# Performance work log

Hardware: AMD Instinct MI355X
Metric: run time of the kernel (lower is better)

The kernel has to match this reference:

```python
import jax, jax.numpy as jnp
import numpy as np

B, T, S = 64, 128, 128
E, H, D, K = 512, 1024, 1024, 1024  # embed, hidden, decoder_size, encoder.output_size
IN2 = 2 * D + 2 * H  # output_rnn input size


def gru_cell(x, h, Wih, Whh, bih, bhh):
    # PyTorch GRUCell math; gate order (r, z, n)
    gi = x @ Wih.T + bih
    gh = h @ Whh.T + bhh
    i_r, i_z, i_n = jnp.split(gi, 3, axis=-1)
    h_r, h_z, h_n = jnp.split(gh, 3, axis=-1)
    r = jax.nn.sigmoid(i_r + h_r)
    z = jax.nn.sigmoid(i_z + h_z)
    n = jnp.tanh(i_n + r * h_n)
    return (1.0 - z) * n + z * h


def setup_inputs() -> dict:
    key = jax.random.key(0)
    ks = jax.random.split(key, 24)
    p = 0.05
    rn = lambda k, s, sc=1.0: jax.random.normal(k, s, jnp.float32) * sc
    return {
        'reversed_input': rn(ks[0], (B, T, E)),
        'y_length': jnp.full((B,), T, jnp.int32),
        'mask': jnp.ones((B, T), bool),
        'y_states': rn(ks[1], (B, T, D)),
        'encoder_output': rn(ks[2], (B, S, K)),
        'src_mask': jnp.ones((B, 1, S), bool),
        # backward-reading GRU (self.rnn)
        'rnn_Wih': rn(ks[3], (3 * H, E), p), 'rnn_Whh': rn(ks[4], (3 * H, H), p),
        'rnn_bih': rn(ks[5], (3 * H,), p), 'rnn_bhh': rn(ks[6], (3 * H,), p),
        # output_rnn GRU
        'out_Wih': rn(ks[7], (3 * H, IN2), p), 'out_Whh': rn(ks[8], (3 * H, H), p),
        'out_bih': rn(ks[9], (3 * H,), p), 'out_bhh': rn(ks[10], (3 * H,), p),
        'corr_W': rn(ks[11], (D, H), p), 'corr_b': rn(ks[12], (D,), p),
        'reward_W': rn(ks[13], (2, H), p), 'reward_b': rn(ks[14], (2,), p),
        'attv_W': rn(ks[15], (H, H + K), p), 'attv_b': rn(ks[16], (H,), p),
        # Bahdanau attention (bias-free linears)
        'key_W': rn(ks[17], (H, K), p), 'query_W': rn(ks[18], (H, H), p),
        'energy_W': rn(ks[19], (1, H), p),
    }


def reference(reversed_input, y_length, mask, y_states, encoder_output, src_mask,
              rnn_Wih, rnn_Whh, rnn_bih, rnn_bhh,
              out_Wih, out_Whh, out_bih, out_bhh,
              corr_W, corr_b, reward_W, reward_b,
              attv_W, attv_b, key_W, query_W, energy_W):
    b, t, _ = reversed_input.shape
    h_dim = rnn_Whh.shape[1]
    d_dim = corr_W.shape[0]
    dt = reversed_input.dtype

    # _apply_rnn: step-by-step GRU over reversed input == full GRU scan
    def rnn_step(h, x):
        h = gru_cell(x, h, rnn_Wih, rnn_Whh, rnn_bih, rnn_bhh)
        return h, h
    h0 = jnp.zeros((b, h_dim), dt)
    _, rnn_outs = jax.lax.scan(rnn_step, h0, reversed_input.transpose(1, 0, 2))
    rnn_outputs = jnp.flip(rnn_outs.transpose(1, 0, 2), axis=1)  # [B,T,H]

    proj_keys = encoder_output @ key_W.T  # [B,S,H] precomputed attention keys
    comb_states = jnp.concatenate([y_states, rnn_outputs], axis=-1)  # [B,T,D+H]
    sm = src_mask[:, 0, :]  # [B,S]

    def step(carry, comb_t):
        h, corr_prev, att_prev = carry
        inp = jnp.concatenate([comb_t, corr_prev, att_prev], axis=-1)  # [B,2D+2H]
        h = gru_cell(inp, h, out_Wih, out_Whh, out_bih, out_bhh)  # rnn_output == hidden[-1]
        corr = jnp.tanh(h @ corr_W.T + corr_b)  # corr_activation=tanh
        reward = h @ reward_W.T + reward_b  # [B,2]
        reward_pred = jax.lax.stop_gradient(jnp.argmax(reward, axis=-1)).astype(dt)[:, None]
        # Bahdanau attention: v^T tanh(Wq q + Wk k)
        pq = h @ query_W.T  # [B,H]
        energies = jnp.tanh(pq[:, None, :] + proj_keys) @ energy_W[0]  # [B,S]
        scores = jnp.where(sm, energies, -jnp.inf)
        alphas = jax.nn.softmax(scores, axis=-1)
        context = jnp.einsum('bs,bsk->bk', alphas, encoder_output)
        att_vec = jnp.tanh(jnp.concatenate([h, context], axis=-1) @ attv_W.T + attv_b)
        corr = corr * (1.0 - reward_pred)
        return (h, corr, att_vec), (corr, reward, alphas)

    init = (jnp.zeros((b, h_dim), dt), jnp.zeros((b, d_dim), dt), jnp.zeros((b, h_dim), dt))
    _, (corrs, rewards, attns) = jax.lax.scan(step, init, comb_states.transpose(1, 0, 2))
    return (corrs.transpose(1, 0, 2), rewards.transpose(1, 0, 2), attns.transpose(1, 0, 2))
```

## Files before the change

kernel.cpp:

```cpp
#include <hip/hip_runtime.h>
#include <hip/hip_bf16.h>
#include <math.h>

#define B 64
#define T 128
#define S 128
#define E 512
#define H 1024
#define D 1024
#define KDIM 1024
#define G3 3072
#define JT 16

__device__ __forceinline__ float sigmoidf_(float x) { return 1.f / (1.f + expf(-x)); }

struct SBSeg { const float* A; const float* W; int lda; int ldw; int N; int colOff; };
struct SBArgs { SBSeg s[6]; };

__global__ __launch_bounds__(256) void sb_gemm(SBArgs args, int jtPerSeg, int Nstr,
                                               float* __restrict__ part) {
  const int seg = blockIdx.x / jtPerSeg;
  const int jt = blockIdx.x % jtPerSeg;
  const SBSeg sg = args.s[seg];
  const int j0 = jt * JT;
  if (j0 >= sg.N) return;
  const int wv = __builtin_amdgcn_readfirstlane(threadIdx.x >> 6);
  const int lane = threadIdx.x & 63;

  float a[128];
  const float4* ap = (const float4*)(sg.A + (size_t)lane * sg.lda + wv * 128);
#pragma unroll
  for (int q = 0; q < 32; ++q) {
    float4 v = ap[q];
    a[q * 4 + 0] = v.x; a[q * 4 + 1] = v.y; a[q * 4 + 2] = v.z; a[q * 4 + 3] = v.w;
  }
  float acc[JT];
#pragma unroll
  for (int jj = 0; jj < JT; ++jj) acc[jj] = 0.f;
#pragma unroll
  for (int jj = 0; jj < JT; ++jj) {
    int j = j0 + jj;
    if (j < sg.N) {
      const float4* wp = (const float4*)(sg.W + (size_t)j * sg.ldw + wv * 128);
      float s0 = 0.f, s1 = 0.f, s2 = 0.f, s3 = 0.f;
#pragma unroll
      for (int q = 0; q < 32; ++q) {
        float4 w4 = wp[q];
        s0 = fmaf(a[q * 4 + 0], w4.x, s0);
        s1 = fmaf(a[q * 4 + 1], w4.y, s1);
        s2 = fmaf(a[q * 4 + 2], w4.z, s2);
        s3 = fmaf(a[q * 4 + 3], w4.w, s3);
      }
      acc[jj] = (s0 + s1) + (s2 + s3);
    }
  }
  __shared__ float red[4][JT][64];
#pragma unroll
  for (int jj = 0; jj < JT; ++jj) red[wv][jj][lane] = acc[jj];
  __syncthreads();
  for (int idx = threadIdx.x; idx < JT * 64; idx += 256) {
    int jj = idx >> 6, b = idx & 63;
    int j = j0 + jj;
    if (j < sg.N) {
      float v = red[0][jj][b] + red[1][jj][b] + red[2][jj][b] + red[3][jj][b];
      part[((size_t)seg * Nstr + sg.colOff + j) * 64 + b] = v;
    }
  }
}

__global__ __launch_bounds__(256) void gru_reduce(
    const float* __restrict__ part, const float* __restrict__ pre_t,
    int giPlanes, int ghStart, int ghPlanes, const float* __restrict__ bhh,
    float* __restrict__ hrow, int hstride, float* __restrict__ flip_out, int t) {
  const int j0 = blockIdx.x * 4;
  const int jj = threadIdx.x >> 6;
  const int b = threadIdx.x & 63;
  const int j = j0 + jj;
  float gir = pre_t[(size_t)j * 64 + b];
  float giz = pre_t[(size_t)(H + j) * 64 + b];
  float gin = pre_t[(size_t)(2 * H + j) * 64 + b];
  for (int p2 = 0; p2 < giPlanes; ++p2) {
    const float* pp = part + (size_t)p2 * G3 * 64;
    gir += pp[(size_t)j * 64 + b];
    giz += pp[(size_t)(H + j) * 64 + b];
    gin += pp[(size_t)(2 * H + j) * 64 + b];
  }
  float ghr = bhh[j], ghz = bhh[H + j], ghn = bhh[2 * H + j];
  for (int p2 = ghStart; p2 < ghStart + ghPlanes; ++p2) {
    const float* pp = part + (size_t)p2 * G3 * 64;
    ghr += pp[(size_t)j * 64 + b];
    ghz += pp[(size_t)(H + j) * 64 + b];
    ghn += pp[(size_t)(2 * H + j) * 64 + b];
  }
  float r = sigmoidf_(gir + ghr);
  float z = sigmoidf_(giz + ghz);
  float n = tanhf(gin + r * ghn);
  float hold = hrow[(size_t)b * hstride + j];
  float hnew = (1.f - z) * n + z * hold;
  __shared__ float st[4][64];
  st[jj][b] = hnew;
  __syncthreads();
  int jl = threadIdx.x & 3, b2 = threadIdx.x >> 2;
  float v = st[jl][b2];
  hrow[(size_t)b2 * hstride + j0 + jl] = v;
  if (flip_out)
    flip_out[(size_t)b2 * T * H + (size_t)(T - 1 - t) * H + j0 + jl] = v;
}

__global__ __launch_bounds__(256) void hproj_reduce(
    const float* __restrict__ part, const float* __restrict__ corr_b,
    const float* __restrict__ reward_b, float* __restrict__ corrT,
    float* __restrict__ rewT, float* __restrict__ pq,
    float* __restrict__ out_rewards, int t) {
  const int j0 = blockIdx.x * 4;
  const int jj = threadIdx.x >> 6;
  const int b = threadIdx.x & 63;
  const int j = j0 + jj;
  __shared__ float st[4][64];
  float v = 0.f;
  if (j < 2050) {
    int p0 = (j < 1024) ? 0 : (j < 1026) ? 2 : 4;
    v = part[((size_t)p0 * 2050 + j) * 64 + b] +
        part[((size_t)(p0 + 1) * 2050 + j) * 64 + b];
    if (j < 1024) {
      corrT[(size_t)j * 64 + b] = v + corr_b[j];
    } else if (j < 1026) {
      int l = j - 1024;
      float rv = v + reward_b[l];
      rewT[l * 64 + b] = rv;
      out_rewards[((size_t)b * T + t) * 2 + l] = rv;
    }
  }
  st[jj][b] = v;
  __syncthreads();
  int jl = threadIdx.x & 3, b2 = threadIdx.x >> 2;
  int jq = j0 + jl;
  if (jq >= 1026 && jq < 2050)
    pq[(size_t)b2 * 1024 + (jq - 1026)] = st[jl][b2];
}

__global__ __launch_bounds__(256) void energy_kernel(
    const float* __restrict__ pq, const float* __restrict__ pk,
    const float* __restrict__ eW, float* __restrict__ energies) {
  int wid = blockIdx.x * 4 + (threadIdx.x >> 6);
  int lane = threadIdx.x & 63;
  int b = wid >> 7, s = wid & 127;
  const float* pkp = pk + ((size_t)b * S + s) * H;
  const float* qp = pq + (size_t)b * H;
  float acc = 0.f;
#pragma unroll
  for (int i = 0; i < 16; ++i) {
    int j = lane + i * 64;
    acc += tanhf(qp[j] + pkp[j]) * eW[j];
  }
#pragma unroll
  for (int off = 32; off > 0; off >>= 1) acc += __shfl_down(acc, off);
  if (lane == 0) energies[b * S + s] = acc;
}

__global__ __launch_bounds__(256) void smct_kernel(
    const float* __restrict__ energies, const float* __restrict__ enc,
    float* __restrict__ hcat, float* __restrict__ out_attn, int t) {
  int b = blockIdx.x, kt = blockIdx.y;
  int tid = threadIdx.x;
  __shared__ float se[128], sa[128], ss[128];
  if (tid < 128) { se[tid] = energies[b * S + tid]; sa[tid] = se[tid]; }
  __syncthreads();
  for (int st2 = 64; st2 > 0; st2 >>= 1) {
    if (tid < st2) sa[tid] = fmaxf(sa[tid], sa[tid + st2]);
    __syncthreads();
  }
  float mx = sa[0];
  __syncthreads();
  if (tid < 128) { sa[tid] = expf(se[tid] - mx); ss[tid] = sa[tid]; }
  __syncthreads();
  for (int st2 = 64; st2 > 0; st2 >>= 1) {
    if (tid < st2) ss[tid] += ss[tid + st2];
    __syncthreads();
  }
  float inv = 1.f / ss[0];
  __syncthreads();
  if (tid < 128) sa[tid] *= inv;
  __syncthreads();
  int k = kt * 256 + tid;
  const float* eb = enc + (size_t)b * S * KDIM;
  float acc = 0.f;
#pragma unroll 4
  for (int s2 = 0; s2 < 128; ++s2) acc = fmaf(sa[s2], eb[(size_t)s2 * KDIM + k], acc);
  hcat[(size_t)b * 2048 + 1024 + k] = acc;
  if (kt == 0 && tid < 128) out_attn[((size_t)b * T + t) * S + tid] = sa[tid];
}

__global__ __launch_bounds__(256) void finalize_kernel(
    const float* __restrict__ partA, const float* __restrict__ attv_b,
    const float* __restrict__ corrT, const float* __restrict__ rewT,
    float* __restrict__ uv, float* __restrict__ out_corrs, int t) {
  const int j0 = blockIdx.x * 4;
  const int jj = threadIdx.x >> 6;
  const int b = threadIdx.x & 63;
  const int j = j0 + jj;
  float av = attv_b[j];
#pragma unroll
  for (int p2 = 0; p2 < 4; ++p2) av += partA[((size_t)p2 * 1024 + j) * 64 + b];
  av = tanhf(av);
  float r0 = rewT[b], r1 = rewT[64 + b];
  float cv = (r1 > r0) ? 0.f : tanhf(corrT[(size_t)j * 64 + b]);
  __shared__ float stA[4][64], stC[4][64];
  stA[jj][b] = av;
  stC[jj][b] = cv;
  __syncthreads();
  int jl = threadIdx.x & 3, b2 = threadIdx.x >> 2;
  uv[(size_t)b2 * 2048 + j0 + jl] = stC[jl][b2];
  uv[(size_t)b2 * 2048 + 1024 + j0 + jl] = stA[jl][b2];
  out_corrs[((size_t)b2 * T + t) * D + j0 + jl] = stC[jl][b2];
}

template<int KSEL>
__global__ __launch_bounds__(256) void gi_pre_kernel(
    const float* __restrict__ A1, const float* __restrict__ A2,
    const float* __restrict__ W, const float* __restrict__ bias,
    float* __restrict__ pre, int c0) {
  const int t = c0 + blockIdx.y;
  const int tloc = blockIdx.y;
  const int bn = blockIdx.x * 64;
  __shared__ __align__(16) float As[16][68];
  __shared__ __align__(16) float Ws[16][68];
  const int tid = threadIdx.x;
  const int tr = tid >> 4, tc = tid & 15;
  float acc[4][4];
#pragma unroll
  for (int i = 0; i < 4; ++i)
#pragma unroll
    for (int j = 0; j < 4; ++j) acc[i][j] = 0.f;
  const int Kd = KSEL ? 2048 : 512;
  const int ldw = KSEL ? 4096 : 512;
  for (int k0 = 0; k0 < Kd; k0 += 16) {
#pragma unroll
    for (int l = 0; l < 4; ++l) {
      int i = tid + l * 256;
      int r = i >> 4, kk = i & 15;
      float va;
      if (KSEL == 0) {
        va = A1[(size_t)r * (T * E) + (size_t)t * E + k0 + kk];
      } else {
        int k = k0 + kk;
        va = (k < 1024) ? A1[(size_t)r * (T * D) + (size_t)t * D + k]
                        : A2[(size_t)r * (T * H) + (size_t)t * H + (k - 1024)];
      }
      As[kk][r] = va;
    }
#pragma unroll
    for (int l = 0; l < 4; ++l) {
      int i = tid + l * 256;
      int c = i >> 4, kk = i & 15;
      Ws[kk][c] = W[(size_t)(bn + c) * ldw + k0 + kk];
    }
    __syncthreads();
#pragma unroll
    for (int kk = 0; kk < 16; ++kk) {
      float4 avv = *(const float4*)&As[kk][tr * 4];
      float4 wvv = *(const float4*)&Ws[kk][tc * 4];
      float aa[4] = {avv.x, avv.y, avv.z, avv.w};
      float ww[4] = {wvv.x, wvv.y, wvv.z, wvv.w};
#pragma unroll
      for (int i = 0; i < 4; ++i)
#pragma unroll
        for (int j = 0; j < 4; ++j)
          acc[i][j] = fmaf(aa[i], ww[j], acc[i][j]);
    }
    __syncthreads();
  }
  float* dst = pre + (size_t)tloc * G3 * 64;
#pragma unroll
  for (int i = 0; i < 4; ++i)
#pragma unroll
    for (int j = 0; j < 4; ++j) {
      int col = bn + tc * 4 + j;
      dst[(size_t)col * 64 + tr * 4 + i] = acc[i][j] + bias[col];
    }
}

__global__ __launch_bounds__(256) void gemm_nt_big(
    const float* __restrict__ A, int sA, const float* __restrict__ W, int sW,
    float* __restrict__ C, int sC, int Kd) {
  __shared__ __align__(16) float As[16][68];
  __shared__ __align__(16) float Ws[16][68];
  const int bm = blockIdx.y * 64;
  const int bn = blockIdx.x * 64;
  const int tid = threadIdx.x;
  const int tr = tid >> 4, tc = tid & 15;
  float acc[4][4];
#pragma unroll
  for (int i = 0; i < 4; ++i)
#pragma unroll
    for (int j = 0; j < 4; ++j) acc[i][j] = 0.f;
  for (int k0 = 0; k0 < Kd; k0 += 16) {
#pragma unroll
    for (int l = 0; l < 4; ++l) {
      int i = tid + l * 256;
      int r = i >> 4, kk = i & 15;
      As[kk][r] = A[(size_t)(bm + r) * sA + k0 + kk];
    }
#pragma unroll
    for (int l = 0; l < 4; ++l) {
      int i = tid + l * 256;
      int c = i >> 4, kk = i & 15;
      Ws[kk][c] = W[(size_t)(bn + c) * sW + k0 + kk];
    }
    __syncthreads();
#pragma unroll
    for (int kk = 0; kk < 16; ++kk) {
      float4 avv = *(const float4*)&As[kk][tr * 4];
      float4 wvv = *(const float4*)&Ws[kk][tc * 4];
      float aa[4] = {avv.x, avv.y, avv.z, avv.w};
      float ww[4] = {wvv.x, wvv.y, wvv.z, wvv.w};
#pragma unroll
      for (int i = 0; i < 4; ++i)
#pragma unroll
        for (int j = 0; j < 4; ++j)
          acc[i][j] = fmaf(aa[i], ww[j], acc[i][j]);
    }
    __syncthreads();
  }
#pragma unroll
  for (int i = 0; i < 4; ++i)
#pragma unroll
    for (int j = 0; j < 4; ++j)
      C[(size_t)(bm + tr * 4 + i) * sC + bn + tc * 4 + j] = acc[i][j];
}

extern "C" void kernel_launch(void* const* d_in, const int* in_sizes, int n_in,
                              void* d_out, int out_size, void* d_ws, size_t ws_size,
                              hipStream_t stream) {
  const float* reversed_input = (const float*)d_in[0];
  const float* y_states = (const float*)d_in[3];
  const float* encoder = (const float*)d_in[4];
  const float* rnn_Wih = (const float*)d_in[6];
  const float* rnn_Whh = (const float*)d_in[7];
  const float* rnn_bih = (const float*)d_in[8];
  const float* rnn_bhh = (const float*)d_in[9];
  const float* out_Wih = (const float*)d_in[10];
  const float* out_Whh = (const float*)d_in[11];
  const float* out_bih = (const float*)d_in[12];
  const float* out_bhh = (const float*)d_in[13];
  const float* corr_W = (const float*)d_in[14];
  const float* corr_b = (const float*)d_in[15];
  const float* reward_W = (const float*)d_in[16];
  const float* reward_b = (const float*)d_in[17];
  const float* attv_W = (const float*)d_in[18];
  const float* attv_b = (const float*)d_in[19];
  const float* key_W = (const float*)d_in[20];
  const float* query_W = (const float*)d_in[21];
  const float* energy_W = (const float*)d_in[22];

  float* out_corrs = (float*)d_out;
  float* out_rewards = out_corrs + (size_t)B * T * D;
  float* out_attns = out_rewards + (size_t)B * T * 2;

  float* p = (float*)d_ws;
  float* rnn_flip = p;  p += (size_t)B * T * H;
  float* proj_keys = p; p += (size_t)B * S * H;
  float* part = p;      p += (size_t)6 * G3 * 64;
  float* hcat = p;      p += (size_t)B * 2048;
  float* uv = p;        p += (size_t)B * 2048;
  float* h1 = p;        p += (size_t)B * H;
  float* pq = p;        p += (size_t)B * H;
  float* corrT = p;     p += (size_t)D * 64;
  float* rewT = p;      p += 128;
  float* energies = p;  p += (size_t)B * S;
  size_t fixedF = (size_t)(p - (float*)d_ws);
  int CH = 8;
  const size_t perT = (size_t)G3 * 64;
  if (ws_size >= (fixedF + 128ull * perT) * 4) CH = 128;
  else if (ws_size >= (fixedF + 64ull * perT) * 4) CH = 64;
  else if (ws_size >= (fixedF + 32ull * perT) * 4) CH = 32;
  else if (ws_size >= (fixedF + 16ull * perT) * 4) CH = 16;
  float* gibuf = p;

  hipMemsetAsync(h1, 0, (size_t)B * H * sizeof(float), stream);
  hipMemsetAsync(hcat, 0, (size_t)B * 2048 * sizeof(float), stream);
  hipMemsetAsync(uv, 0, (size_t)B * 2048 * sizeof(float), stream);

  dim3 blk(256);

  gemm_nt_big<<<dim3(H / 64, (B * S) / 64), blk, 0, stream>>>(
      encoder, KDIM, key_W, KDIM, proj_keys, H, KDIM);

  for (int c0 = 0; c0 < T; c0 += CH) {
    gi_pre_kernel<0><<<dim3(G3 / 64, CH), blk, 0, stream>>>(
        reversed_input, nullptr, rnn_Wih, rnn_bih, gibuf, c0);
    for (int tl = 0; tl < CH; ++tl) {
      int t = c0 + tl;
      SBArgs s1{};
      s1.s[0] = { h1, rnn_Whh, H, H, G3, 0 };
      s1.s[1] = { h1 + 512, rnn_Whh + 512, H, H, G3, 0 };
      sb_gemm<<<2 * 192, blk, 0, stream>>>(s1, 192, G3, part);
      gru_reduce<<<256, blk, 0, stream>>>(part, gibuf + (size_t)tl * perT,
                                          0, 0, 2, rnn_bhh, h1, H, rnn_flip, t);
    }
  }

  for (int c0 = 0; c0 < T; c0 += CH) {
    gi_pre_kernel<1><<<dim3(G3 / 64, CH), blk, 0, stream>>>(
        y_states, rnn_flip, out_Wih, out_bih, gibuf, c0);
    for (int tl = 0; tl < CH; ++tl) {
      int t = c0 + tl;
      SBArgs k1{};
      for (int s2 = 0; s2 < 4; ++s2)
        k1.s[s2] = { uv + s2 * 512, out_Wih + 2048 + s2 * 512, 2048, 4096, G3, 0 };
      for (int s2 = 0; s2 < 2; ++s2)
        k1.s[4 + s2] = { hcat + s2 * 512, out_Whh + s2 * 512, 2048, H, G3, 0 };
      sb_gemm<<<6 * 192, blk, 0, stream>>>(k1, 192, G3, part);
      gru_reduce<<<256, blk, 0, stream>>>(part, gibuf + (size_t)tl * perT,
                                          4, 4, 2, out_bhh, hcat, 2048, nullptr, t);
      SBArgs hp{};
      hp.s[0] = { hcat, corr_W, 2048, H, 1024, 0 };
      hp.s[1] = { hcat + 512, corr_W + 512, 2048, H, 1024, 0 };
      hp.s[2] = { hcat, reward_W, 2048, H, 2, 1024 };
      hp.s[3] = { hcat + 512, reward_W + 512, 2048, H, 2, 1024 };
      hp.s[4] = { hcat, query_W, 2048, H, 1024, 1026 };
      hp.s[5] = { hcat + 512, query_W + 512, 2048, H, 1024, 1026 };
      sb_gemm<<<6 * 64, blk, 0, stream>>>(hp, 64, 2050, part);
      hproj_reduce<<<513, blk, 0, stream>>>(part, corr_b, reward_b, corrT, rewT,
                                            pq, out_rewards, t);
      energy_kernel<<<2048, blk, 0, stream>>>(pq, proj_keys, energy_W, energies);
      smct_kernel<<<dim3(B, 4), blk, 0, stream>>>(energies, encoder, hcat, out_attns, t);
      SBArgs av{};
      for (int s2 = 0; s2 < 4; ++s2)
        av.s[s2] = { hcat + s2 * 512, attv_W + s2 * 512, 2048, 2048, 1024, 0 };
      sb_gemm<<<4 * 64, blk, 0, stream>>>(av, 64, 1024, part + (size_t)6 * 2050 * 64);
      finalize_kernel<<<256, blk, 0, stream>>>(part + (size_t)6 * 2050 * 64, attv_b,
                                               corrT, rewT, uv, out_corrs, t);
    }
  }
}
```

Measured before the change: 23.32 ms.

## Fuse attention chain per batch row and split attv GEMM into h and ctx parts

Result: slower. 57.21 ms (+145.4%).

```diff
diff --git a/kernel.cpp b/kernel.cpp
--- a/kernel.cpp
+++ b/kernel.cpp
@@ -11,11 +11,12 @@
 #define KDIM 1024
 #define G3 3072
 #define JT 16
+#define NSTR 3074
 
 __device__ __forceinline__ float sigmoidf_(float x) { return 1.f / (1.f + expf(-x)); }
 
 struct SBSeg { const float* A; const float* W; int lda; int ldw; int N; int colOff; };
-struct SBArgs { SBSeg s[6]; };
+struct SBArgs { SBSeg s[8]; };
 
 __global__ __launch_bounds__(256) void sb_gemm(SBArgs args, int jtPerSeg, int Nstr,
                                                float* __restrict__ part) {
@@ -107,112 +108,135 @@
     flip_out[(size_t)b2 * T * H + (size_t)(T - 1 - t) * H + j0 + jl] = v;
 }
 
-__global__ __launch_bounds__(256) void hproj_reduce(
-    const float* __restrict__ part, const float* __restrict__ corr_b,
-    const float* __restrict__ reward_b, float* __restrict__ corrT,
-    float* __restrict__ rewT, float* __restrict__ pq,
-    float* __restrict__ out_rewards, int t) {
-  const int j0 = blockIdx.x * 4;
-  const int jj = threadIdx.x >> 6;
-  const int b = threadIdx.x & 63;
-  const int j = j0 + jj;
-  __shared__ float st[4][64];
-  float v = 0.f;
-  if (j < 2050) {
-    int p0 = (j < 1024) ? 0 : (j < 1026) ? 2 : 4;
-    v = part[((size_t)p0 * 2050 + j) * 64 + b] +
-        part[((size_t)(p0 + 1) * 2050 + j) * 64 + b];
-    if (j < 1024) {
-      corrT[(size_t)j * 64 + b] = v + corr_b[j];
-    } else if (j < 1026) {
-      int l = j - 1024;
-      float rv = v + reward_b[l];
-      rewT[l * 64 + b] = rv;
-      out_rewards[((size_t)b * T + t) * 2 + l] = rv;
-    }
-  }
-  st[jj][b] = v;
-  __syncthreads();
-  int jl = threadIdx.x & 3, b2 = threadIdx.x >> 2;
-  int jq = j0 + jl;
-  if (jq >= 1026 && jq < 2050)
-    pq[(size_t)b2 * 1024 + (jq - 1026)] = st[jl][b2];
-}
-
-__global__ __launch_bounds__(256) void energy_kernel(
-    const float* __restrict__ pq, const float* __restrict__ pk,
-    const float* __restrict__ eW, float* __restrict__ energies) {
-  int wid = blockIdx.x * 4 + (threadIdx.x >> 6);
-  int lane = threadIdx.x & 63;
-  int b = wid >> 7, s = wid & 127;
-  const float* pkp = pk + ((size_t)b * S + s) * H;
-  const float* qp = pq + (size_t)b * H;
-  float acc = 0.f;
-#pragma unroll
-  for (int i = 0; i < 16; ++i) {
-    int j = lane + i * 64;
-    acc += tanhf(qp[j] + pkp[j]) * eW[j];
-  }
-#pragma unroll
-  for (int off = 32; off > 0; off >>= 1) acc += __shfl_down(acc, off);
-  if (lane == 0) energies[b * S + s] = acc;
-}
-
-__global__ __launch_bounds__(256) void smct_kernel(
-    const float* __restrict__ energies, const float* __restrict__ enc,
-    float* __restrict__ hcat, float* __restrict__ out_attn, int t) {
-  int b = blockIdx.x, kt = blockIdx.y;
-  int tid = threadIdx.x;
-  __shared__ float se[128], sa[128], ss[128];
-  if (tid < 128) { se[tid] = energies[b * S + tid]; sa[tid] = se[tid]; }
-  __syncthreads();
-  for (int st2 = 64; st2 > 0; st2 >>= 1) {
-    if (tid < st2) sa[tid] = fmaxf(sa[tid], sa[tid + st2]);
-    __syncthreads();
-  }
-  float mx = sa[0];
-  __syncthreads();
-  if (tid < 128) { sa[tid] = expf(se[tid] - mx); ss[tid] = sa[tid]; }
-  __syncthreads();
-  for (int st2 = 64; st2 > 0; st2 >>= 1) {
-    if (tid < st2) ss[tid] += ss[tid + st2];
-    __syncthreads();
-  }
-  float inv = 1.f / ss[0];
-  __syncthreads();
-  if (tid < 128) sa[tid] *= inv;
-  __syncthreads();
-  int k = kt * 256 + tid;
-  const float* eb = enc + (size_t)b * S * KDIM;
-  float acc = 0.f;
+__global__ __launch_bounds__(256) void attn_fused(
+    const float* __restrict__ part, const float* __restrict__ pk,
+    const float* __restrict__ eW, const float* __restrict__ enc,
+    const float* __restrict__ reward_b,
+    float* __restrict__ ctx, float* __restrict__ rewgate,
+    float* __restrict__ out_rewards, float* __restrict__ out_attns, int t) {
+  const int b = blockIdx.x;
+  const int tid = threadIdx.x;
+  const int wv = tid >> 6, lane = tid & 63;
+  __shared__ float pqs[1024];
+  __shared__ float al[128], tmp[128];
+  __shared__ float rg[2];
+  for (int j = tid; j < 1024; j += 256)
+    pqs[j] = part[((size_t)4 * NSTR + 1026 + j) * 64 + b] +
+             part[((size_t)5 * NSTR + 1026 + j) * 64 + b];
+  if (tid < 2) {
+    float rv = part[((size_t)2 * NSTR + 1024 + tid) * 64 + b] +
+               part[((size_t)3 * NSTR + 1024 + tid) * 64 + b] + reward_b[tid];
+    out_rewards[((size_t)b * T + t) * 2 + tid] = rv;
+    rg[tid] = rv;
+  }
+  __syncthreads();
+  for (int s = wv; s < S; s += 4) {
+    const float* pkp = pk + ((size_t)b * S + s) * H;
+    float acc = 0.f;
+#pragma unroll
+    for (int i = 0; i < 16; ++i) {
+      int j = lane + i * 64;
+      acc += tanhf(pqs[j] + pkp[j]) * eW[j];
+    }
+#pragma unroll
+    for (int off = 32; off > 0; off >>= 1) acc += __shfl_down(acc, off);
+    if (lane == 0) al[s] = acc;
+  }
+  __syncthreads();
+  if (tid < 128) tmp[tid] = al[tid];
+  __syncthreads();
+  for (int st = 64; st > 0; st >>= 1) {
+    if (tid < st) tmp[tid] = fmaxf(tmp[tid], tmp[tid + st]);
+    __syncthreads();
+  }
+  float mx = tmp[0];
+  __syncthreads();
+  float e = 0.f;
+  if (tid < 128) { e = expf(al[tid] - mx); tmp[tid] = e; }
+  __syncthreads();
+  for (int st = 64; st > 0; st >>= 1) {
+    if (tid < st) tmp[tid] += tmp[tid + st];
+    __syncthreads();
+  }
+  float inv = 1.f / tmp[0];
+  __syncthreads();
+  if (tid < 128) {
+    float a2 = e * inv;
+    al[tid] = a2;
+    out_attns[((size_t)b * T + t) * S + tid] = a2;
+  }
+  __syncthreads();
+  for (int k = tid; k < KDIM; k += 256) {
+    const float* eb = enc + (size_t)b * S * KDIM + k;
+    float acc = 0.f;
 #pragma unroll 4
-  for (int s2 = 0; s2 < 128; ++s2) acc = fmaf(sa[s2], eb[(size_t)s2 * KDIM + k], acc);
-  hcat[(size_t)b * 2048 + 1024 + k] = acc;
-  if (kt == 0 && tid < 128) out_attn[((size_t)b * T + t) * S + tid] = sa[tid];
-}
-
-__global__ __launch_bounds__(256) void finalize_kernel(
-    const float* __restrict__ partA, const float* __restrict__ attv_b,
-    const float* __restrict__ corrT, const float* __restrict__ rewT,
+    for (int s2 = 0; s2 < S; ++s2) acc = fmaf(al[s2], eb[(size_t)s2 * KDIM], acc);
+    ctx[(size_t)b * KDIM + k] = acc;
+  }
+  if (tid == 0) rewgate[b] = (rg[1] > rg[0]) ? 0.f : 1.f;
+}
+
+__global__ __launch_bounds__(256) void final_kernel(
+    const float* __restrict__ part, const float* __restrict__ avW,
+    const float* __restrict__ avB, const float* __restrict__ corr_b,
+    const float* __restrict__ ctx, const float* __restrict__ rewgate,
     float* __restrict__ uv, float* __restrict__ out_corrs, int t) {
-  const int j0 = blockIdx.x * 4;
-  const int jj = threadIdx.x >> 6;
-  const int b = threadIdx.x & 63;
-  const int j = j0 + jj;
-  float av = attv_b[j];
-#pragma unroll
-  for (int p2 = 0; p2 < 4; ++p2) av += partA[((size_t)p2 * 1024 + j) * 64 + b];
-  av = tanhf(av);
-  float r0 = rewT[b], r1 = rewT[64 + b];
-  float cv = (r1 > r0) ? 0.f : tanhf(corrT[(size_t)j * 64 + b]);
-  __shared__ float stA[4][64], stC[4][64];
-  stA[jj][b] = av;
-  stC[jj][b] = cv;
-  __syncthreads();
-  int jl = threadIdx.x & 3, b2 = threadIdx.x >> 2;
-  uv[(size_t)b2 * 2048 + j0 + jl] = stC[jl][b2];
-  uv[(size_t)b2 * 2048 + 1024 + j0 + jl] = stA[jl][b2];
-  out_corrs[((size_t)b2 * T + t) * D + j0 + jl] = stC[jl][b2];
+  const int blk = blockIdx.x;
+  const int tid = threadIdx.x;
+  if (blk < 64) {
+    const int wv = tid >> 6, lane = tid & 63;
+    const int n0 = blk * 16;
+    __shared__ float red[4][16][64];
+    float acc[16];
+#pragma unroll
+    for (int jj = 0; jj < 16; ++jj) acc[jj] = 0.f;
+    const float* arow = ctx + (size_t)lane * KDIM + wv * 256;
+    for (int sc = 0; sc < 8; ++sc) {
+      float av[32];
+      const float4* ap = (const float4*)(arow + sc * 32);
+#pragma unroll
+      for (int q = 0; q < 8; ++q) {
+        float4 v = ap[q];
+        av[4*q] = v.x; av[4*q+1] = v.y; av[4*q+2] = v.z; av[4*q+3] = v.w;
+      }
+#pragma unroll
+      for (int jj = 0; jj < 16; ++jj) {
+        const float4* wp = (const float4*)(avW + (size_t)(n0 + jj) * 2048 + 1024 + wv * 256 + sc * 32);
+        float s = acc[jj];
+#pragma unroll
+        for (int q = 0; q < 8; ++q) {
+          float4 w = wp[q];
+          s = fmaf(av[4*q],   w.x, s);
+          s = fmaf(av[4*q+1], w.y, s);
+          s = fmaf(av[4*q+2], w.z, s);
+          s = fmaf(av[4*q+3], w.w, s);
+        }
+        acc[jj] = s;
+      }
+    }
+#pragma unroll
+    for (int jj = 0; jj < 16; ++jj) red[wv][jj][lane] = acc[jj];
+    __syncthreads();
+    for (int idx = tid; idx < 1024; idx += 256) {
+      int jj = idx >> 6, bb = idx & 63;
+      int n = n0 + jj;
+      float v = red[0][jj][bb] + red[1][jj][bb] + red[2][jj][bb] + red[3][jj][bb]
+              + part[((size_t)6 * NSTR + 2050 + n) * 64 + bb]
+              + part[((size_t)7 * NSTR + 2050 + n) * 64 + bb] + avB[n];
+      uv[(size_t)bb * 2048 + 1024 + n] = tanhf(v);
+    }
+  } else {
+    const int j0 = (blk - 64) * 8;
+    for (int idx = tid; idx < 512; idx += 256) {
+      int jj = idx >> 6, bb = idx & 63;
+      int j = j0 + jj;
+      float v = part[((size_t)0 * NSTR + j) * 64 + bb] +
+                part[((size_t)1 * NSTR + j) * 64 + bb] + corr_b[j];
+      float cv = rewgate[bb] * tanhf(v);
+      uv[(size_t)bb * 2048 + j] = cv;
+      out_corrs[((size_t)bb * T + t) * D + j] = cv;
+    }
+  }
 }
 
 template<int KSEL>
@@ -360,25 +384,19 @@
   float* p = (float*)d_ws;
   float* rnn_flip = p;  p += (size_t)B * T * H;
   float* proj_keys = p; p += (size_t)B * S * H;
-  float* part = p;      p += (size_t)6 * G3 * 64;
-  float* hcat = p;      p += (size_t)B * 2048;
+  float* part = p;      p += (size_t)8 * NSTR * 64;
+  float* h = p;         p += (size_t)B * H;
   float* uv = p;        p += (size_t)B * 2048;
-  float* h1 = p;        p += (size_t)B * H;
-  float* pq = p;        p += (size_t)B * H;
-  float* corrT = p;     p += (size_t)D * 64;
-  float* rewT = p;      p += 128;
-  float* energies = p;  p += (size_t)B * S;
+  float* ctx = p;       p += (size_t)B * KDIM;
+  float* rewgate = p;   p += 64;
   size_t fixedF = (size_t)(p - (float*)d_ws);
+  const size_t perT = (size_t)G3 * 64;
   int CH = 8;
-  const size_t perT = (size_t)G3 * 64;
-  if (ws_size >= (fixedF + 128ull * perT) * 4) CH = 128;
-  else if (ws_size >= (fixedF + 64ull * perT) * 4) CH = 64;
-  else if (ws_size >= (fixedF + 32ull * perT) * 4) CH = 32;
+  if (ws_size >= (fixedF + 32ull * perT) * 4) CH = 32;
   else if (ws_size >= (fixedF + 16ull * perT) * 4) CH = 16;
   float* gibuf = p;
 
-  hipMemsetAsync(h1, 0, (size_t)B * H * sizeof(float), stream);
-  hipMemsetAsync(hcat, 0, (size_t)B * 2048 * sizeof(float), stream);
+  hipMemsetAsync(h, 0, (size_t)B * H * sizeof(float), stream);
   hipMemsetAsync(uv, 0, (size_t)B * 2048 * sizeof(float), stream);
 
   dim3 blk(256);
@@ -392,14 +410,15 @@
     for (int tl = 0; tl < CH; ++tl) {
       int t = c0 + tl;
       SBArgs s1{};
-      s1.s[0] = { h1, rnn_Whh, H, H, G3, 0 };
-      s1.s[1] = { h1 + 512, rnn_Whh + 512, H, H, G3, 0 };
+      s1.s[0] = { h, rnn_Whh, H, H, G3, 0 };
+      s1.s[1] = { h + 512, rnn_Whh + 512, H, H, G3, 0 };
       sb_gemm<<<2 * 192, blk, 0, stream>>>(s1, 192, G3, part);
       gru_reduce<<<256, blk, 0, stream>>>(part, gibuf + (size_t)tl * perT,
-                                          0, 0, 2, rnn_bhh, h1, H, rnn_flip, t);
-    }
-  }
-
+                                          0, 0, 2, rnn_bhh, h, H, rnn_flip, t);
+    }
+  }
+
+  hipMemsetAsync(h, 0, (size_t)B * H * sizeof(float), stream);
   for (int c0 = 0; c0 < T; c0 += CH) {
     gi_pre_kernel<1><<<dim3(G3 / 64, CH), blk, 0, stream>>>(
         y_states, rnn_flip, out_Wih, out_bih, gibuf, c0);
@@ -409,28 +428,25 @@
       for (int s2 = 0; s2 < 4; ++s2)
         k1.s[s2] = { uv + s2 * 512, out_Wih + 2048 + s2 * 512, 2048, 4096, G3, 0 };
       for (int s2 = 0; s2 < 2; ++s2)
-        k1.s[4 + s2] = { hcat + s2 * 512, out_Whh + s2 * 512, 2048, H, G3, 0 };
+        k1.s[4 + s2] = { h + s2 * 512, out_Whh + s2 * 512, H, H, G3, 0 };
       sb_gemm<<<6 * 192, blk, 0, stream>>>(k1, 192, G3, part);
       gru_reduce<<<256, blk, 0, stream>>>(part, gibuf + (size_t)tl * perT,
-                                          4, 4, 2, out_bhh, hcat, 2048, nullptr, t);
+                                          4, 4, 2, out_bhh, h, H, nullptr, t);
       SBArgs hp{};
-      hp.s[0] = { hcat, corr_W, 2048, H, 1024, 0 };
-      hp.s[1] = { hcat + 512, corr_W + 512, 2048, H, 1024, 0 };
-      hp.s[2] = { hcat, reward_W, 2048, H, 2, 1024 };
-      hp.s[3] = { hcat + 512, reward_W + 512, 2048, H, 2, 1024 };
-      hp.s[4] = { hcat, query_W, 2048, H, 1024, 1026 };
-      hp.s[5] = { hcat + 512, query_W + 512, 2048, H, 1024, 1026 };
-      sb_gemm<<<6 * 64, blk, 0, stream>>>(hp, 64, 2050, part);
-      hproj_reduce<<<513, blk, 0, stream>>>(part, corr_b, reward_b, corrT, rewT,
-                                            pq, out_rewards, t);
-      energy_kernel<<<2048, blk, 0, stream>>>(pq, proj_keys, energy_W, energies);
-      smct_kernel<<<dim3(B, 4), blk, 0, stream>>>(energies, encoder, hcat, out_attns, t);
-      SBArgs av{};
-      for (int s2 = 0; s2 < 4; ++s2)
-        av.s[s2] = { hcat + s2 * 512, attv_W + s2 * 512, 2048, 2048, 1024, 0 };
-      sb_gemm<<<4 * 64, blk, 0, stream>>>(av, 64, 1024, part + (size_t)6 * 2050 * 64);
-      finalize_kernel<<<256, blk, 0, stream>>>(part + (size_t)6 * 2050 * 64, attv_b,
-                                               corrT, rewT, uv, out_corrs, t);
-    }
-  }
-}
+      hp.s[0] = { h, corr_W, H, H, 1024, 0 };
+      hp.s[1] = { h + 512, corr_W + 512, H, H, 1024, 0 };
+      hp.s[2] = { h, reward_W, H, H, 2, 1024 };
+      hp.s[3] = { h + 512, reward_W + 512, H, H, 2, 1024 };
+      hp.s[4] = { h, query_W, H, H, 1024, 1026 };
+      hp.s[5] = { h + 512, query_W + 512, H, H, 1024, 1026 };
+      hp.s[6] = { h, attv_W, H, 2048, 1024, 2050 };
+      hp.s[7] = { h + 512, attv_W + 512, H, 2048, 1024, 2050 };
+      sb_gemm<<<8 * 64, blk, 0, stream>>>(hp, 64, NSTR, part);
+      attn_fused<<<64, blk, 0, stream>>>(part, proj_keys, energy_W, encoder,
+                                         reward_b, ctx, rewgate,
+                                         out_rewards, out_attns, t);
+      final_kernel<<<192, blk, 0, stream>>>(part, attv_W, attv_b, corr_b, ctx,
+                                            rewgate, uv, out_corrs, t);
+    }
+  }
+}
```
